# Kernel tuning notes

Measured on AMD Instinct MI355X. Metric: run time of the kernel, lower is better.

The kernel has to match this reference:

```python
import jax, jax.numpy as jnp
import numpy as np

B, H, W = 8, 640, 640
NUM_INST = 16  # upper bound on instance ids; segment reduce handles absent ids


def _bce(p, t):
    # torch BCELoss clamps log terms at -100
    lp = jnp.clip(jnp.log(p), -100.0)
    l1p = jnp.clip(jnp.log1p(-p), -100.0)
    return -(t * lp + (1.0 - t) * l1p)


def setup_inputs() -> dict:
    key = jax.random.key(0)
    k1, k2, k3, k4 = jax.random.split(key, 4)
    preds = jax.random.uniform(k1, (B, 2, H, W), dtype=jnp.float32,
                               minval=1e-4, maxval=1.0 - 1e-4)
    conf = jax.random.bernoulli(k2, 0.3, (B, H, W)).astype(jnp.float32)
    overlap = jax.random.bernoulli(k3, 0.1, (B, H, W)).astype(jnp.float32)
    inst = jax.random.randint(k4, (B, H, W), 0, NUM_INST, dtype=jnp.int32)
    inds = jnp.arange(B, dtype=jnp.int64) if jax.config.jax_enable_x64 else jnp.arange(B, dtype=jnp.int32)
    return {"preds": preds, "conf": conf, "inst": inst,
            "overlap": overlap, "inds": inds}


def reference(preds, conf, inst, overlap, inds):
    p1 = preds[:, 0]
    p2 = preds[:, 1]
    and_preds = p1 * p2
    and_loss_map = _bce(and_preds, overlap)            # [B,H,W]
    or_loss = _bce(jnp.maximum(p1, p2), conf).mean()
    and_overlap = and_preds * overlap
    op1 = jnp.maximum(p1, and_overlap)
    op2 = jnpp = jnp.maximum(p2, and_overlap)

    b, h, w = p1.shape
    # per-(sample, instance-id) segment reduce replacing the python loops.
    # MSELoss(bop*mask, mask)/sum(mask) == segment-mean of (op-1)^2 over the mask.
    seg = (jnp.arange(b, dtype=jnp.int32)[:, None, None] * NUM_INST + inst).reshape(-1)
    e1 = ((op1 - 1.0) ** 2).reshape(-1)
    e2 = ((op2 - 1.0) ** 2).reshape(-1)
    nseg = b * NUM_INST
    cnt = jax.ops.segment_sum(jnp.ones_like(e1), seg, num_segments=nseg).reshape(b, NUM_INST)
    s1 = jax.ops.segment_sum(e1, seg, num_segments=nseg).reshape(b, NUM_INST)
    s2 = jax.ops.segment_sum(e2, seg, num_segments=nseg).reshape(b, NUM_INST)
    present = cnt > 0
    safe_cnt = jnp.where(present, cnt, 1.0)
    d1 = s1 / safe_cnt
    d2 = s2 / safe_cnt
    # min(d1,d2) - max(d1,d2) + 1 == 1 - |d1 - d2|, only for present keys
    per_key = jnp.where(present, 1.0 - jnp.abs(d1 - d2), 0.0)
    nkeys = present.sum(axis=1).astype(p1.dtype)       # torch.unique count per sample
    inst_loss = (per_key.sum(axis=1) / nkeys).mean()

    pos = (conf == 1).astype(p1.dtype)
    neg = (conf == 0).astype(p1.dtype)
    and_loss = (and_loss_map * pos).sum() / pos.sum() + (and_loss_map * neg).sum() / neg.sum()

    return 0.5 * and_loss + 0.25 * or_loss + 0.25 * inst_loss
```

## Files before the change

### kernel.cpp

```cpp
#include <hip/hip_runtime.h>
#include <hip/hip_bf16.h>

#define BB 8
#define HH 640
#define WW 640
#define HWN (HH * WW)
#define NUM_INST 16
#define NBLK 128
#define NBLK_TOT (NBLK * BB)
#define THREADS 256
#define NV 36


__device__ __forceinline__ void process_pixel(
    float p1, float p2, float c, float t, int k,
    float* s12, unsigned* cnt_s,
    float& lgPos, float& lgAll, float& lgOr, float& accCnt)
{
    float andp = p1 * p2;
    bool tpos = (t != 0.0f);
    bool cpos = (c != 0.0f);
    float argA = tpos ? andp : (1.0f - andp);
    float lg = __logf(argA);
    lgAll += lg;
    lgPos = fmaf(c, lg, lgPos);
    accCnt += c;
    float mx = fmaxf(p1, p2);
    float argO = cpos ? mx : (1.0f - mx);
    lgOr += __logf(argO);
    float ao = t * andp;
    float d1 = fmaxf(p1, ao) - 1.0f;
    float d2 = fmaxf(p2, ao) - 1.0f;
    float e12 = (d1 - d2) * (d1 + d2);
    #pragma unroll
    for (int j = 0; j < NUM_INST; ++j) {
        bool m = (k == j);
        s12[j] += m ? e12 : 0.0f;
        cnt_s[j] += (unsigned)__popcll(__ballot(m));
    }
}

__global__ __launch_bounds__(THREADS) void overlap_main_kernel(
    const float* __restrict__ preds, const float* __restrict__ conf,
    const int* __restrict__ inst, const float* __restrict__ overlap,
    float* __restrict__ ws)
{
    const int b   = blockIdx.y;
    const int tid = threadIdx.x;

    const float4* p1v = (const float4*)(preds + (size_t)b * 2 * HWN);
    const float4* p2v = (const float4*)(preds + (size_t)b * 2 * HWN + HWN);
    const float4* cv  = (const float4*)(conf    + (size_t)b * HWN);
    const float4* tv  = (const float4*)(overlap + (size_t)b * HWN);
    const int4*   kv  = (const int4*)(inst      + (size_t)b * HWN);

    float s12[NUM_INST];
    unsigned cnt_s[NUM_INST];
    #pragma unroll
    for (int j = 0; j < NUM_INST; ++j) { s12[j] = 0.0f; cnt_s[j] = 0u; }
    float lgPos = 0.0f, lgAll = 0.0f, lgOr = 0.0f, accCnt = 0.0f;

    const int nvec   = HWN / 4;
    const int stride = NBLK * THREADS;
    for (int i = blockIdx.x * THREADS + tid; i < nvec; i += stride) {
        float4 A = p1v[i];
        float4 B = p2v[i];
        float4 C = cv[i];
        float4 T = tv[i];
        int4   K = kv[i];
        process_pixel(A.x, B.x, C.x, T.x, K.x, s12, cnt_s, lgPos, lgAll, lgOr, accCnt);
        process_pixel(A.y, B.y, C.y, T.y, K.y, s12, cnt_s, lgPos, lgAll, lgOr, accCnt);
        process_pixel(A.z, B.z, C.z, T.z, K.z, s12, cnt_s, lgPos, lgAll, lgOr, accCnt);
        process_pixel(A.w, B.w, C.w, T.w, K.w, s12, cnt_s, lgPos, lgAll, lgOr, accCnt);
    }

    float fv[20];
    #pragma unroll
    for (int j = 0; j < NUM_INST; ++j) fv[j] = s12[j];
    fv[16] = lgPos; fv[17] = lgAll; fv[18] = lgOr; fv[19] = accCnt;
    #pragma unroll
    for (int s = 32; s > 0; s >>= 1) {
        #pragma unroll
        for (int v = 0; v < 20; ++v) fv[v] += __shfl_xor(fv[v], s, 64);
    }

    __shared__ float wsum[4][NV];
    const int wave = tid >> 6;
    const int lane = tid & 63;
    if (lane == 0) {
        #pragma unroll
        for (int j = 0; j < NUM_INST; ++j) {
            wsum[wave][j]      = fv[j];
            wsum[wave][16 + j] = (float)cnt_s[j];
        }
        wsum[wave][32] = -fv[16];
        wsum[wave][33] = -fv[17];
        wsum[wave][34] = -fv[18];
        wsum[wave][35] = fv[19];
    }
    __syncthreads();
    if (tid < NV) {
        float s = wsum[0][tid] + wsum[1][tid] + wsum[2][tid] + wsum[3][tid];
        int g = blockIdx.y * NBLK + blockIdx.x;
        ws[tid * NBLK_TOT + g] = s;
    }
}

__global__ __launch_bounds__(320) void overlap_finalize_kernel(
    const float* __restrict__ ws, float* __restrict__ out)
{
    __shared__ float seg[BB][NV];
    __shared__ float perkey[BB][NUM_INST];
    __shared__ float pres[BB][NUM_INST];
    __shared__ float binst[BB];
    const int t = threadIdx.x;

    if (t < BB * NV) {
        int b = t / NV, v = t - (t / NV) * NV;
        const float4* p = (const float4*)(ws + v * NBLK_TOT + b * NBLK);
        float4 s4 = {0.0f, 0.0f, 0.0f, 0.0f};
        #pragma unroll 8
        for (int i = 0; i < NBLK / 4; ++i) {
            float4 q = p[i];
            s4.x += q.x; s4.y += q.y; s4.z += q.z; s4.w += q.w;
        }
        seg[b][v] = (s4.x + s4.y) + (s4.z + s4.w);
    }
    __syncthreads();

    if (t < BB * NUM_INST) {
        int b = t >> 4, k = t & 15;
        float c = seg[b][16 + k];
        bool present = c > 0.0f;
        float sc = present ? c : 1.0f;
        perkey[b][k] = present ? (1.0f - fabsf(seg[b][k]) / sc) : 0.0f;
        pres[b][k]   = present ? 1.0f : 0.0f;
    }
    __syncthreads();

    if (t < BB) {
        float s = 0.0f, nk = 0.0f;
        for (int k = 0; k < NUM_INST; ++k) { s += perkey[t][k]; nk += pres[t][k]; }
        binst[t] = s / nk;
    }
    __syncthreads();

    if (t == 0) {
        float instLoss = 0.0f, posS = 0.0f, allS = 0.0f, orS = 0.0f, posC = 0.0f;
        for (int b = 0; b < BB; ++b) {
            instLoss += binst[b];
            posS += seg[b][32];
            allS += seg[b][33];
            orS  += seg[b][34];
            posC += seg[b][35];
        }
        instLoss *= (1.0f / (float)BB);
        const float N = (float)BB * (float)HWN;
        float negS = allS - posS;
        float andLoss = posS / posC + negS / (N - posC);
        float orLoss  = orS / N;
        out[0] = 0.5f * andLoss + 0.25f * orLoss + 0.25f * instLoss;
    }
}

extern "C" void kernel_launch(void* const* d_in, const int* in_sizes, int n_in,
                              void* d_out, int out_size, void* d_ws, size_t ws_size,
                              hipStream_t stream) {
    const float* preds   = (const float*)d_in[0];
    const float* conf    = (const float*)d_in[1];
    const int*   inst    = (const int*)d_in[2];
    const float* overlap = (const float*)d_in[3];
    float* ws  = (float*)d_ws;
    float* out = (float*)d_out;

    dim3 grid(NBLK, BB);
    overlap_main_kernel<<<grid, THREADS, 0, stream>>>(preds, conf, inst, overlap, ws);
    overlap_finalize_kernel<<<1, 320, 0, stream>>>(ws, out);
}
```

Measured before the change: 109.9 us.

## Replace per-pixel ballot counting with packed nibble histograms, use log2, unroll grid loop

Instance counts were previously gathered with 16 ballot+popcount operations per pixel. They are now accumulated as packed 4-bit counters in two 64-bit registers, which are unpacked into 16-bit lanes and reduced with wave shuffles at the end. Logs switch to __log2f, and the sum is rescaled by ln2 once per wave instead of per pixel. The strided loop becomes a fixed, fully unrolled sequence of four iterations, which relies on the hardcoded problem size so that each nibble stays below overflow.

```diff
diff --git a/kernel.cpp b/kernel.cpp
--- a/kernel.cpp
+++ b/kernel.cpp
@@ -10,34 +10,54 @@
 #define NBLK_TOT (NBLK * BB)
 #define THREADS 256
 #define NV 36
+#define LN2F 0.69314718055994530942f
 
 
 __device__ __forceinline__ void process_pixel(
     float p1, float p2, float c, float t, int k,
-    float* s12, unsigned* cnt_s,
+    float* s12, unsigned long long& h,
     float& lgPos, float& lgAll, float& lgOr, float& accCnt)
 {
     float andp = p1 * p2;
     bool tpos = (t != 0.0f);
     bool cpos = (c != 0.0f);
     float argA = tpos ? andp : (1.0f - andp);
-    float lg = __logf(argA);
+    float lg = __log2f(argA);
     lgAll += lg;
     lgPos = fmaf(c, lg, lgPos);
     accCnt += c;
     float mx = fmaxf(p1, p2);
     float argO = cpos ? mx : (1.0f - mx);
-    lgOr += __logf(argO);
+    lgOr += __log2f(argO);
     float ao = t * andp;
-    float d1 = fmaxf(p1, ao) - 1.0f;
-    float d2 = fmaxf(p2, ao) - 1.0f;
-    float e12 = (d1 - d2) * (d1 + d2);
+    float a  = fmaxf(p1, ao);
+    float b2 = fmaxf(p2, ao);
+    float e12 = (a - b2) * ((a + b2) - 2.0f);
+    h += 1ull << (k << 2);
     #pragma unroll
     for (int j = 0; j < NUM_INST; ++j) {
         bool m = (k == j);
         s12[j] += m ? e12 : 0.0f;
-        cnt_s[j] += (unsigned)__popcll(__ballot(m));
-    }
+    }
+}
+
+__device__ __forceinline__ void process_vec4(
+    int i,
+    const float4* __restrict__ p1v, const float4* __restrict__ p2v,
+    const float4* __restrict__ cv,  const float4* __restrict__ tv,
+    const int4*   __restrict__ kv,
+    float* s12, unsigned long long& h,
+    float& lgPos, float& lgAll, float& lgOr, float& accCnt)
+{
+    float4 A = p1v[i];
+    float4 B = p2v[i];
+    float4 C = cv[i];
+    float4 T = tv[i];
+    int4   K = kv[i];
+    process_pixel(A.x, B.x, C.x, T.x, K.x, s12, h, lgPos, lgAll, lgOr, accCnt);
+    process_pixel(A.y, B.y, C.y, T.y, K.y, s12, h, lgPos, lgAll, lgOr, accCnt);
+    process_pixel(A.z, B.z, C.z, T.z, K.z, s12, h, lgPos, lgAll, lgOr, accCnt);
+    process_pixel(A.w, B.w, C.w, T.w, K.w, s12, h, lgPos, lgAll, lgOr, accCnt);
 }
 
 __global__ __launch_bounds__(THREADS) void overlap_main_kernel(
@@ -55,23 +75,27 @@
     const int4*   kv  = (const int4*)(inst      + (size_t)b * HWN);
 
     float s12[NUM_INST];
-    unsigned cnt_s[NUM_INST];
-    #pragma unroll
-    for (int j = 0; j < NUM_INST; ++j) { s12[j] = 0.0f; cnt_s[j] = 0u; }
+    #pragma unroll
+    for (int j = 0; j < NUM_INST; ++j) s12[j] = 0.0f;
+    unsigned long long h0 = 0ull, h1 = 0ull;
     float lgPos = 0.0f, lgAll = 0.0f, lgOr = 0.0f, accCnt = 0.0f;
 
     const int nvec   = HWN / 4;
     const int stride = NBLK * THREADS;
-    for (int i = blockIdx.x * THREADS + tid; i < nvec; i += stride) {
-        float4 A = p1v[i];
-        float4 B = p2v[i];
-        float4 C = cv[i];
-        float4 T = tv[i];
-        int4   K = kv[i];
-        process_pixel(A.x, B.x, C.x, T.x, K.x, s12, cnt_s, lgPos, lgAll, lgOr, accCnt);
-        process_pixel(A.y, B.y, C.y, T.y, K.y, s12, cnt_s, lgPos, lgAll, lgOr, accCnt);
-        process_pixel(A.z, B.z, C.z, T.z, K.z, s12, cnt_s, lgPos, lgAll, lgOr, accCnt);
-        process_pixel(A.w, B.w, C.w, T.w, K.w, s12, cnt_s, lgPos, lgAll, lgOr, accCnt);
+    int i = blockIdx.x * THREADS + tid;
+    process_vec4(i, p1v, p2v, cv, tv, kv, s12, h0, lgPos, lgAll, lgOr, accCnt); i += stride;
+    process_vec4(i, p1v, p2v, cv, tv, kv, s12, h0, lgPos, lgAll, lgOr, accCnt); i += stride;
+    process_vec4(i, p1v, p2v, cv, tv, kv, s12, h1, lgPos, lgAll, lgOr, accCnt); i += stride;
+    if (i < nvec)
+        process_vec4(i, p1v, p2v, cv, tv, kv, s12, h1, lgPos, lgAll, lgOr, accCnt);
+
+    unsigned ev[8];
+    #pragma unroll
+    for (int q = 0; q < 4; ++q) {
+        unsigned long long e = ((h0 >> (4 * q)) & 0x000F000F000F000FULL)
+                             + ((h1 >> (4 * q)) & 0x000F000F000F000FULL);
+        ev[2 * q]     = (unsigned)e;
+        ev[2 * q + 1] = (unsigned)(e >> 32);
     }
 
     float fv[20];
@@ -82,6 +106,8 @@
     for (int s = 32; s > 0; s >>= 1) {
         #pragma unroll
         for (int v = 0; v < 20; ++v) fv[v] += __shfl_xor(fv[v], s, 64);
+        #pragma unroll
+        for (int e = 0; e < 8; ++e) ev[e] += (unsigned)__shfl_xor((int)ev[e], s, 64);
     }
 
     __shared__ float wsum[4][NV];
@@ -89,13 +115,17 @@
     const int lane = tid & 63;
     if (lane == 0) {
         #pragma unroll
-        for (int j = 0; j < NUM_INST; ++j) {
-            wsum[wave][j]      = fv[j];
-            wsum[wave][16 + j] = (float)cnt_s[j];
+        for (int j = 0; j < NUM_INST; ++j) wsum[wave][j] = fv[j];
+        #pragma unroll
+        for (int k = 0; k < NUM_INST; ++k) {
+            int q = k & 3, f = k >> 2;
+            unsigned w = ev[2 * q + (f >> 1)];
+            unsigned cnt = (w >> (16 * (f & 1))) & 0xFFFFu;
+            wsum[wave][16 + k] = (float)cnt;
         }
-        wsum[wave][32] = -fv[16];
-        wsum[wave][33] = -fv[17];
-        wsum[wave][34] = -fv[18];
+        wsum[wave][32] = -LN2F * fv[16];
+        wsum[wave][33] = -LN2F * fv[17];
+        wsum[wave][34] = -LN2F * fv[18];
         wsum[wave][35] = fv[19];
     }
     __syncthreads();
```

New measurement: 111.5 us. About the same (+1.4%).
